# Performance work log

Hardware: AMD Instinct MI355X
Metric: run time of the kernel (lower is better)

Reference implementation:

```python
import jax, jax.numpy as jnp
import numpy as np


def _vieta_pell_basis(x, degree):
    # Iterative recurrence: V0 = 2, V1 = x, Vn = x*V_{n-1} + V_{n-2}
    basis = [2.0 * jnp.ones_like(x), x]
    for _ in range(2, degree + 1):
        basis.append(x * basis[-1] + basis[-2])
    return jnp.stack(basis[: degree + 1], axis=-1)  # [b, i, d+1]


def setup_inputs() -> dict:
    key = jax.random.key(0)
    k1, k2 = jax.random.split(key)
    batch, input_dim, output_dim, degree = 4096, 1024, 1024, 8
    x = jax.random.normal(k1, (batch, input_dim), dtype=jnp.float32)
    std = 1.0 / (input_dim * (degree + 1))
    vp_coeffs = jax.random.normal(k2, (input_dim, output_dim, degree + 1), dtype=jnp.float32) * std
    return {"x": x, "vp_coeffs": vp_coeffs}


def reference(x, vp_coeffs):
    degree = vp_coeffs.shape[-1] - 1
    xt = jnp.tanh(x)  # [b, i]
    vp_basis = _vieta_pell_basis(xt, degree)  # [b, i, d+1]
    y = jnp.einsum("bid,iod->bo", vp_basis, vp_coeffs)
    return y
```

## Files before the change

### kernel.cpp

```cpp
#include <hip/hip_runtime.h>
#include <hip/hip_bf16.h>

typedef unsigned short u16;
typedef unsigned int   u32;
typedef unsigned long long u64;

#define BATCH 4096
#define IDIM  1024
#define ODIM  1024
#define NDEG  9
#define KA    8192
#define NZ    4
#define KZ    (KA / NZ)
#define GBK   64
#define NT    (KZ / GBK)

typedef __attribute__((ext_vector_type(8))) short short8_t;
typedef __attribute__((ext_vector_type(4))) float f32x4;

__device__ __forceinline__ u16 f2bf(float f) {
    union { float f; u32 u; } v; v.f = f;
    u32 r = v.u + 0x7FFFu + ((v.u >> 16) & 1u);
    return (u16)(r >> 16);
}
__device__ __forceinline__ u32 pack2bf(float lo, float hi) {
    return (u32)f2bf(lo) | ((u32)f2bf(hi) << 16);
}
__device__ __forceinline__ float bf2f(u16 h) {
    union { u32 u; float f; } v; v.u = (u32)h << 16; return v.f;
}

__device__ __forceinline__ void gl_lds16(const u16* g, u16* l) {
    __builtin_amdgcn_global_load_lds(
        (const __attribute__((address_space(1))) void*)g,
        (__attribute__((address_space(3))) void*)l,
        16, 0, 0);
}

#define BARRIER()   __builtin_amdgcn_s_barrier()
#define WAIT_LGKM0() do { asm volatile("s_waitcnt lgkmcnt(0)" ::: "memory"); \
                          __builtin_amdgcn_sched_barrier(0); } while (0)
#define WAIT_VM8()  asm volatile("s_waitcnt vmcnt(8)" ::: "memory")
#define WAIT_VM0()  asm volatile("s_waitcnt vmcnt(0)" ::: "memory")

#define PB_TI 128
#define PB_TO 8
#define PB_J  (PB_TO * NDEG)
#define PB_LS 132

#define NB_B   1024
#define NB_A   2048

__global__ void prep_kernel(const float* __restrict__ x,
                            const float* __restrict__ c,
                            u16* __restrict__ A, u16* __restrict__ Bt,
                            float* __restrict__ Pr) {
    __shared__ u16 lds[PB_J * PB_LS];
    const int bb  = blockIdx.x;
    const int tid = threadIdx.x;

    if (bb < NB_B) {
        const int i0 = (bb & 7) * PB_TI;
        const int o0 = (bb >> 3) * PB_TO;
        const float* src = c + (size_t)i0 * (ODIM * NDEG) + (size_t)o0 * NDEG;
#pragma unroll
        for (int t = 0; t < 36; ++t) {
            int f  = t * 256 + tid;
            int ii = f / PB_J;
            int j  = f - ii * PB_J;
            float v = src[(size_t)ii * (ODIM * NDEG) + j];
            lds[j * PB_LS + ii] = f2bf(v);
        }
        __syncthreads();

        {
            int o   = tid >> 5;
            int sub = tid & 31;
            const u16* row = lds + (o * NDEG) * PB_LS + sub * 4;
            float s = bf2f(row[0]) + bf2f(row[1]) + bf2f(row[2]) + bf2f(row[3]);
#pragma unroll
            for (int m = 16; m >= 1; m >>= 1)
                s += __shfl_xor(s, m, 64);
            if (sub == 0)
                Pr[(size_t)(bb & 7) * ODIM + o0 + o] = s;
        }

#pragma unroll
        for (int t = 0; t < 9; ++t) {
            int g   = t * 256 + tid;
            int j   = g >> 5;
            int ii4 = (g & 31) << 2;
            int o   = j / NDEG;
            int d   = j - o * NDEG;
            if (d != 0) {
                u64 v = *(const u64*)(lds + j * PB_LS + ii4);
                *(u64*)(Bt + (size_t)(o0 + o) * KA + (d - 1) * 1024 + i0 + ii4) = v;
            }
        }
    } else {
        int t  = (bb - NB_B) * 256 + tid;
        int b  = t >> 7;
        int i8 = (t & 127) << 3;
        const float4* xv = (const float4*)(x + ((size_t)t << 3));
        float4 xa = xv[0], xb = xv[1];
        float th[8] = {tanhf(xa.x), tanhf(xa.y), tanhf(xa.z), tanhf(xa.w),
                       tanhf(xb.x), tanhf(xb.y), tanhf(xb.z), tanhf(xb.w)};
        float va[8], vb[8];
#pragma unroll
        for (int j = 0; j < 8; ++j) { va[j] = 2.0f; vb[j] = th[j]; }
        u16* dst = A + (size_t)b * KA + i8;
        uint4 w;
        w.x = pack2bf(th[0], th[1]); w.y = pack2bf(th[2], th[3]);
        w.z = pack2bf(th[4], th[5]); w.w = pack2bf(th[6], th[7]);
        *(uint4*)dst = w;
#pragma unroll
        for (int d = 2; d < NDEG; ++d) {
            float nx[8];
#pragma unroll
            for (int j = 0; j < 8; ++j) {
                nx[j] = th[j] * vb[j] + va[j];
                va[j] = vb[j]; vb[j] = nx[j];
            }
            w.x = pack2bf(nx[0], nx[1]); w.y = pack2bf(nx[2], nx[3]);
            w.z = pack2bf(nx[4], nx[5]); w.w = pack2bf(nx[6], nx[7]);
            *(uint4*)(dst + (size_t)(d - 1) * 1024) = w;
        }
    }
}

#define MFMA_QUAD(MH, NH)                                                      \
    __builtin_amdgcn_s_setprio(1);                                            \
    _Pragma("unroll")                                                         \
    for (int kk = 0; kk < 2; ++kk)                                            \
        _Pragma("unroll")                                                     \
        for (int m = 0; m < 4; ++m)                                           \
            _Pragma("unroll")                                                 \
            for (int n = 0; n < 2; ++n)                                       \
                acc[(MH) * 4 + m][(NH) * 2 + n] =                             \
                    __builtin_amdgcn_mfma_f32_16x16x32_bf16(                  \
                        af[m][kk], bf[NH][n][kk],                             \
                        acc[(MH) * 4 + m][(NH) * 2 + n], 0, 0, 0);            \
    __builtin_amdgcn_s_setprio(0);

__global__ __launch_bounds__(512, 2)
void gemm_kernel(const u16* __restrict__ A, const u16* __restrict__ B,
                 float* __restrict__ P, float* __restrict__ out) {
    __shared__ __align__(16) u16 ldsA[2][16384];
    __shared__ __align__(16) u16 ldsB[2][16384];

    const int tid  = threadIdx.x;
    const int lane = tid & 63;
    const int wave = tid >> 6;
    const int quad = lane >> 4;
    const int l15  = lane & 15;
    const int wm   = wave >> 2;
    const int wn   = wave & 3;

    const int bid = blockIdx.x;
    const int z   = bid >> 6;
    const int loc = bid & 63;
    const int swz = (loc & 7) * 8 + (loc >> 3);
    const int bm  = swz >> 2;
    const int bn  = swz & 3;
    const int kStart = z * KZ;

    const u16* gA[4]; const u16* gB[4];
#pragma unroll
    for (int i = 0; i < 4; ++i) {
        int s  = i * 512 + tid;
        int r  = s >> 3;
        int sc = (s & 7) ^ (r & 7);
        gA[i] = A + (size_t)(bm * 256 + r) * KA + kStart + sc * 8;
        gB[i] = B + (size_t)(bn * 256 + r) * KA + kStart + sc * 8;
    }

    f32x4 acc[8][4];
#pragma unroll
    for (int i = 0; i < 8; ++i)
#pragma unroll
        for (int j = 0; j < 4; ++j)
            acc[i][j] = (f32x4){0.f, 0.f, 0.f, 0.f};

#pragma unroll
    for (int i = 0; i < 4; ++i) gl_lds16(gA[i], &ldsA[0][i * 4096 + tid * 8]);
#pragma unroll
    for (int i = 0; i < 4; ++i) gl_lds16(gB[i], &ldsB[0][i * 4096 + tid * 8]);
#pragma unroll
    for (int i = 0; i < 4; ++i) gl_lds16(gA[i] + GBK, &ldsA[1][i * 4096 + tid * 8]);
#pragma unroll
    for (int i = 0; i < 4; ++i) gl_lds16(gB[i] + GBK, &ldsB[1][i * 4096 + tid * 8]);
#pragma unroll
    for (int i = 0; i < 4; ++i) { gA[i] += 2 * GBK; gB[i] += 2 * GBK; }
    WAIT_VM8();
    BARRIER();

    const int pc0  = quad ^ (l15 & 7);
    const int pc1  = (4 + quad) ^ (l15 & 7);
    const int offA = (wm * 128 + l15) * 64;
    const int offB = (wn * 32 + l15) * 64;

    short8_t af[4][2], bf[2][2][2];

    for (int t = 0; t < NT; ++t) {
        const u16* lA = ldsA[t & 1];
        const u16* lB = ldsB[t & 1];
        u16* sA = &ldsA[t & 1][tid * 8];
        u16* sB = &ldsB[t & 1][tid * 8];
        const bool pf = (t + 2 < NT);

#pragma unroll
        for (int m = 0; m < 4; ++m) {
            af[m][0] = *(const short8_t*)(lA + offA + m * 1024 + pc0 * 8);
            af[m][1] = *(const short8_t*)(lA + offA + m * 1024 + pc1 * 8);
        }
#pragma unroll
        for (int nh = 0; nh < 2; ++nh)
#pragma unroll
            for (int n = 0; n < 2; ++n) {
                bf[nh][n][0] = *(const short8_t*)(lB + offB + nh * 8192 + n * 1024 + pc0 * 8);
                bf[nh][n][1] = *(const short8_t*)(lB + offB + nh * 8192 + n * 1024 + pc1 * 8);
            }
        BARRIER();
        WAIT_LGKM0();
        MFMA_QUAD(0, 0);
        BARRIER();

        if (pf) {
            gl_lds16(gA[0], sA);
            gl_lds16(gA[2], sA + 8192);
            gl_lds16(gB[0], sB);
            gl_lds16(gB[1], sB + 4096);
            gl_lds16(gB[2], sB + 8192);
            gl_lds16(gB[3], sB + 12288);
        }
        MFMA_QUAD(0, 1);
        BARRIER();

#pragma unroll
        for (int m = 0; m < 4; ++m) {
            af[m][0] = *(const short8_t*)(lA + offA + 4096 + m * 1024 + pc0 * 8);
            af[m][1] = *(const short8_t*)(lA + offA + 4096 + m * 1024 + pc1 * 8);
        }
        BARRIER();
        WAIT_LGKM0();
        MFMA_QUAD(1, 1);
        BARRIER();

        if (pf) {
            gl_lds16(gA[1], sA + 4096);
            gl_lds16(gA[3], sA + 12288);
        }
        MFMA_QUAD(1, 0);
        if (pf) {
            WAIT_VM8();
#pragma unroll
            for (int i = 0; i < 4; ++i) { gA[i] += GBK; gB[i] += GBK; }
        } else if (t + 1 < NT) {
            WAIT_VM0();
        }
        BARRIER();
    }

    float* C = (z == 0) ? out : P + (size_t)(z - 1) * (BATCH * ODIM);
#pragma unroll
    for (int mh = 0; mh < 2; ++mh)
#pragma unroll
        for (int m = 0; m < 4; ++m)
#pragma unroll
            for (int nh = 0; nh < 2; ++nh)
#pragma unroll
                for (int n = 0; n < 2; ++n) {
                    int row0 = bm * 256 + wm * 128 + mh * 64 + m * 16 + quad * 4;
                    int col  = bn * 256 + nh * 128 + wn * 32 + n * 16 + l15;
#pragma unroll
                    for (int r = 0; r < 4; ++r)
                        C[(size_t)(row0 + r) * ODIM + col] = acc[mh * 4 + m][nh * 2 + n][r];
                }
}

__global__ void reduce_kernel(const float* __restrict__ P,
                              const float* __restrict__ Pr,
                              float* __restrict__ out) {
    int t  = blockIdx.x * 256 + threadIdx.x;
    int o4 = t & 255;
    f32x4 a = ((const f32x4*)out)[t];
    a += ((const f32x4*)P)[t];
    a += ((const f32x4*)(P + (size_t)BATCH * ODIM))[t];
    a += ((const f32x4*)(P + 2 * (size_t)BATCH * ODIM))[t];
    f32x4 r = (f32x4){0.f, 0.f, 0.f, 0.f};
#pragma unroll
    for (int blk = 0; blk < 8; ++blk)
        r += ((const f32x4*)Pr)[blk * 256 + o4];
    ((f32x4*)out)[t] = a + r + r;
}

extern "C" void kernel_launch(void* const* d_in, const int* in_sizes, int n_in,
                              void* d_out, int out_size, void* d_ws, size_t ws_size,
                              hipStream_t stream) {
    const float* x      = (const float*)d_in[0];
    const float* coeffs = (const float*)d_in[1];
    float* out = (float*)d_out;
    (void)ws_size;

    u16*   A  = (u16*)d_ws;
    u16*   Bt = A + (size_t)BATCH * KA;
    float* Pr = (float*)(Bt + (size_t)ODIM * KA);
    float* P  = Pr + 8 * ODIM;

    prep_kernel<<<NB_B + NB_A, 256, 0, stream>>>(x, coeffs, A, Bt, Pr);
    gemm_kernel<<<256, 512, 0, stream>>>(A, Bt, P, out);
    reduce_kernel<<<BATCH * ODIM / 1024, 256, 0, stream>>>(P, Pr, out);
}
```

Baseline: 188.6 us.

## Restructure GEMM main loop into four-phase interleaved LDS read and prefetch schedule

The GEMM main loop becomes four phases per K-tile. Each phase reads a smaller A/B fragment set from LDS (B fragments cut from 2x2x2 to 2x2), issues two global-to-LDS stage loads for upcoming tiles, waits, and runs one MFMA quadrant. Prefetch loads are spread more evenly across phases, and register pressure from B fragments drops. The cost is re-reading A and B fragments from LDS each phase, which adds LDS traffic, plus a tighter vmcnt wait schedule that must stay correct with the partial-tile staging order.

```diff
diff --git a/kernel.cpp b/kernel.cpp
--- a/kernel.cpp
+++ b/kernel.cpp
@@ -40,7 +40,8 @@
 #define BARRIER()   __builtin_amdgcn_s_barrier()
 #define WAIT_LGKM0() do { asm volatile("s_waitcnt lgkmcnt(0)" ::: "memory"); \
                           __builtin_amdgcn_sched_barrier(0); } while (0)
-#define WAIT_VM8()  asm volatile("s_waitcnt vmcnt(8)" ::: "memory")
+#define WAIT_LGKM8() asm volatile("s_waitcnt lgkmcnt(8)" ::: "memory")
+#define WAIT_VM4()  asm volatile("s_waitcnt vmcnt(4)" ::: "memory")
 #define WAIT_VM0()  asm volatile("s_waitcnt vmcnt(0)" ::: "memory")
 
 #define PB_TI 128
@@ -128,7 +129,78 @@
     }
 }
 
-#define MFMA_QUAD(MH, NH)                                                      \
+__global__ __launch_bounds__(512, 2)
+void gemm_kernel(const u16* __restrict__ A, const u16* __restrict__ B,
+                 float* __restrict__ P, float* __restrict__ out) {
+    __shared__ __align__(16) u16 ldsA[2][16384];
+    __shared__ __align__(16) u16 ldsB[2][16384];
+
+    const int tid  = threadIdx.x;
+    const int lane = tid & 63;
+    const int wave = tid >> 6;
+    const int quad = lane >> 4;
+    const int l15  = lane & 15;
+    const int wm   = wave >> 2;
+    const int wn   = wave & 3;
+
+    const int bid = blockIdx.x;
+    const int z   = bid >> 6;
+    const int loc = bid & 63;
+    const int swz = (loc & 7) * 8 + (loc >> 3);
+    const int bm  = swz >> 2;
+    const int bn  = swz & 3;
+    const int kStart = z * KZ;
+
+    const u16* gA[4]; const u16* gB[4];
+#pragma unroll
+    for (int i = 0; i < 4; ++i) {
+        int s  = i * 512 + tid;
+        int r  = s >> 3;
+        int sc = (s & 7) ^ (r & 7);
+        gA[i] = A + (size_t)(bm * 256 + r) * KA + kStart + sc * 8;
+        gB[i] = B + (size_t)(bn * 256 + r) * KA + kStart + sc * 8;
+    }
+
+    f32x4 acc[8][4];
+#pragma unroll
+    for (int i = 0; i < 8; ++i)
+#pragma unroll
+        for (int j = 0; j < 4; ++j)
+            acc[i][j] = (f32x4){0.f, 0.f, 0.f, 0.f};
+
+#define STAGE_A(i, w) gl_lds16(gA[i] + (size_t)(w) * GBK, \
+                               &ldsA[(w) & 1][(i) * 4096 + tid * 8])
+#define STAGE_B(i, w) gl_lds16(gB[i] + (size_t)(w) * GBK, \
+                               &ldsB[(w) & 1][(i) * 4096 + tid * 8])
+
+#pragma unroll
+    for (int i = 0; i < 4; ++i) { STAGE_A(i, 0); STAGE_B(i, 0); }
+    STAGE_A(0, 1); STAGE_A(2, 1); STAGE_B(2, 1); STAGE_B(3, 1);
+    WAIT_VM4();
+    BARRIER();
+
+    const int pc0  = quad ^ (l15 & 7);
+    const int pc1  = (4 + quad) ^ (l15 & 7);
+    const int rowA0 = wm * 128 + l15;
+    const int rowB0 = wn * 32 + l15;
+
+    short8_t af[4][2], bfq[2][2];
+
+#define READ_A(lA, MH)                                                        \
+    _Pragma("unroll")                                                         \
+    for (int m = 0; m < 4; ++m) {                                             \
+        int ro = (rowA0 + (MH) * 64 + m * 16) * 64;                           \
+        af[m][0] = *(const short8_t*)((lA) + ro + pc0 * 8);                   \
+        af[m][1] = *(const short8_t*)((lA) + ro + pc1 * 8);                   \
+    }
+#define READ_B(lB, NH)                                                        \
+    _Pragma("unroll")                                                         \
+    for (int n = 0; n < 2; ++n) {                                             \
+        int ro = (rowB0 + (NH) * 128 + n * 16) * 64;                          \
+        bfq[n][0] = *(const short8_t*)((lB) + ro + pc0 * 8);                  \
+        bfq[n][1] = *(const short8_t*)((lB) + ro + pc1 * 8);                  \
+    }
+#define MFMA_Q(MH, NH)                                                        \
     __builtin_amdgcn_s_setprio(1);                                            \
     _Pragma("unroll")                                                         \
     for (int kk = 0; kk < 2; ++kk)                                            \
@@ -138,126 +210,48 @@
             for (int n = 0; n < 2; ++n)                                       \
                 acc[(MH) * 4 + m][(NH) * 2 + n] =                             \
                     __builtin_amdgcn_mfma_f32_16x16x32_bf16(                  \
-                        af[m][kk], bf[NH][n][kk],                             \
+                        af[m][kk], bfq[n][kk],                                \
                         acc[(MH) * 4 + m][(NH) * 2 + n], 0, 0, 0);            \
     __builtin_amdgcn_s_setprio(0);
-
-__global__ __launch_bounds__(512, 2)
-void gemm_kernel(const u16* __restrict__ A, const u16* __restrict__ B,
-                 float* __restrict__ P, float* __restrict__ out) {
-    __shared__ __align__(16) u16 ldsA[2][16384];
-    __shared__ __align__(16) u16 ldsB[2][16384];
-
-    const int tid  = threadIdx.x;
-    const int lane = tid & 63;
-    const int wave = tid >> 6;
-    const int quad = lane >> 4;
-    const int l15  = lane & 15;
-    const int wm   = wave >> 2;
-    const int wn   = wave & 3;
-
-    const int bid = blockIdx.x;
-    const int z   = bid >> 6;
-    const int loc = bid & 63;
-    const int swz = (loc & 7) * 8 + (loc >> 3);
-    const int bm  = swz >> 2;
-    const int bn  = swz & 3;
-    const int kStart = z * KZ;
-
-    const u16* gA[4]; const u16* gB[4];
-#pragma unroll
-    for (int i = 0; i < 4; ++i) {
-        int s  = i * 512 + tid;
-        int r  = s >> 3;
-        int sc = (s & 7) ^ (r & 7);
-        gA[i] = A + (size_t)(bm * 256 + r) * KA + kStart + sc * 8;
-        gB[i] = B + (size_t)(bn * 256 + r) * KA + kStart + sc * 8;
-    }
-
-    f32x4 acc[8][4];
-#pragma unroll
-    for (int i = 0; i < 8; ++i)
-#pragma unroll
-        for (int j = 0; j < 4; ++j)
-            acc[i][j] = (f32x4){0.f, 0.f, 0.f, 0.f};
-
-#pragma unroll
-    for (int i = 0; i < 4; ++i) gl_lds16(gA[i], &ldsA[0][i * 4096 + tid * 8]);
-#pragma unroll
-    for (int i = 0; i < 4; ++i) gl_lds16(gB[i], &ldsB[0][i * 4096 + tid * 8]);
-#pragma unroll
-    for (int i = 0; i < 4; ++i) gl_lds16(gA[i] + GBK, &ldsA[1][i * 4096 + tid * 8]);
-#pragma unroll
-    for (int i = 0; i < 4; ++i) gl_lds16(gB[i] + GBK, &ldsB[1][i * 4096 + tid * 8]);
-#pragma unroll
-    for (int i = 0; i < 4; ++i) { gA[i] += 2 * GBK; gB[i] += 2 * GBK; }
-    WAIT_VM8();
-    BARRIER();
-
-    const int pc0  = quad ^ (l15 & 7);
-    const int pc1  = (4 + quad) ^ (l15 & 7);
-    const int offA = (wm * 128 + l15) * 64;
-    const int offB = (wn * 32 + l15) * 64;
-
-    short8_t af[4][2], bf[2][2][2];
 
     for (int t = 0; t < NT; ++t) {
         const u16* lA = ldsA[t & 1];
         const u16* lB = ldsB[t & 1];
-        u16* sA = &ldsA[t & 1][tid * 8];
-        u16* sB = &ldsB[t & 1][tid * 8];
-        const bool pf = (t + 2 < NT);
-
-#pragma unroll
-        for (int m = 0; m < 4; ++m) {
-            af[m][0] = *(const short8_t*)(lA + offA + m * 1024 + pc0 * 8);
-            af[m][1] = *(const short8_t*)(lA + offA + m * 1024 + pc1 * 8);
-        }
-#pragma unroll
-        for (int nh = 0; nh < 2; ++nh)
-#pragma unroll
-            for (int n = 0; n < 2; ++n) {
-                bf[nh][n][0] = *(const short8_t*)(lB + offB + nh * 8192 + n * 1024 + pc0 * 8);
-                bf[nh][n][1] = *(const short8_t*)(lB + offB + nh * 8192 + n * 1024 + pc1 * 8);
-            }
+        const bool s1 = (t + 1 < NT);
+        const bool s2 = (t + 2 < NT);
+
+        READ_A(lA, 0); READ_B(lB, 0);
+        if (s1) { STAGE_A(1, t + 1); STAGE_A(3, t + 1); }
+        WAIT_LGKM8();
         BARRIER();
         WAIT_LGKM0();
-        MFMA_QUAD(0, 0);
-        BARRIER();
-
-        if (pf) {
-            gl_lds16(gA[0], sA);
-            gl_lds16(gA[2], sA + 8192);
-            gl_lds16(gB[0], sB);
-            gl_lds16(gB[1], sB + 4096);
-            gl_lds16(gB[2], sB + 8192);
-            gl_lds16(gB[3], sB + 12288);
-        }
-        MFMA_QUAD(0, 1);
-        BARRIER();
-
-#pragma unroll
-        for (int m = 0; m < 4; ++m) {
-            af[m][0] = *(const short8_t*)(lA + offA + 4096 + m * 1024 + pc0 * 8);
-            af[m][1] = *(const short8_t*)(lA + offA + 4096 + m * 1024 + pc1 * 8);
-        }
+        MFMA_Q(0, 0);
+        BARRIER();
+
+        READ_A(lA, 0); READ_B(lB, 1);
+        if (s1) { STAGE_B(0, t + 1); STAGE_B(1, t + 1); }
+        WAIT_LGKM8();
         BARRIER();
         WAIT_LGKM0();
-        MFMA_QUAD(1, 1);
-        BARRIER();
-
-        if (pf) {
-            gl_lds16(gA[1], sA + 4096);
-            gl_lds16(gA[3], sA + 12288);
-        }
-        MFMA_QUAD(1, 0);
-        if (pf) {
-            WAIT_VM8();
-#pragma unroll
-            for (int i = 0; i < 4; ++i) { gA[i] += GBK; gB[i] += GBK; }
-        } else if (t + 1 < NT) {
-            WAIT_VM0();
-        }
+        MFMA_Q(0, 1);
+        BARRIER();
+
+        READ_A(lA, 1); READ_B(lB, 1);
+        if (s2) { STAGE_A(0, t + 2); STAGE_A(2, t + 2); }
+        WAIT_LGKM8();
+        BARRIER();
+        WAIT_LGKM0();
+        MFMA_Q(1, 1);
+        BARRIER();
+
+        READ_A(lA, 1); READ_B(lB, 0);
+        if (s2) { STAGE_B(2, t + 2); STAGE_B(3, t + 2); }
+        WAIT_LGKM8();
+        BARRIER();
+        WAIT_LGKM0();
+        MFMA_Q(1, 0);
+        if (s2)       WAIT_VM4();
+        else if (s1)  WAIT_VM0();
         BARRIER();
     }
 
```

Measured after the change: 200.0 us. +6.0%, slower.
